# Kernel optimization log

Hardware: AMD Instinct MI355X
Metric: run time of the kernel (lower is better)

## Reference

```python
import jax, jax.numpy as jnp
import numpy as np

B, NQ, NK, D_EQUI, D_INV, D_MSG, D_FF, D_OUT = 2, 768, 768, 256, 256, 32, 128, 64


def setup_inputs() -> dict:
    key = jax.random.key(0)
    ks = jax.random.split(key, 14)
    s = 0.05  # weight init scale
    inp = {
        'q_equi': jax.random.normal(ks[0], (B, NQ, 3, D_EQUI), dtype=jnp.float32),
        'q_inv': jax.random.normal(ks[1], (B, NQ, D_INV), dtype=jnp.float32),
        'k_equi': jax.random.normal(ks[2], (B, NK, 3, D_EQUI), dtype=jnp.float32),
        'k_inv': jax.random.normal(ks[3], (B, NK, D_INV), dtype=jnp.float32),
        # projection params (stored [in, out]; torch Linear is [out, in])
        'Wqi': jax.random.normal(ks[4], (D_INV, D_MSG), dtype=jnp.float32) * s,
        'bqi': jnp.zeros((D_MSG,), jnp.float32),
        'Wki': jax.random.normal(ks[5], (D_INV, D_MSG), dtype=jnp.float32) * s,
        'bki': jnp.zeros((D_MSG,), jnp.float32),
        'Wqe': jax.random.normal(ks[6], (D_EQUI, D_MSG), dtype=jnp.float32) * s,
        'bqe': jnp.zeros((D_MSG,), jnp.float32),
        'Wke': jax.random.normal(ks[7], (D_EQUI, D_MSG), dtype=jnp.float32) * s,
        'bke': jnp.zeros((D_MSG,), jnp.float32),
        # message MLP: in_feats = 4*d_message (q_inv, k_inv, dotprods, dists)
        'W1': jax.random.normal(ks[8], (4 * D_MSG, D_FF), dtype=jnp.float32) * s,
        'b1': jnp.zeros((D_FF,), jnp.float32),
        'W2': jax.random.normal(ks[9], (D_FF, D_OUT), dtype=jnp.float32) * s,
        'b2': jnp.zeros((D_OUT,), jnp.float32),
    }
    return inp


def reference(q_equi, q_inv, k_equi, k_inv, Wqi, bqi, Wki, bki, Wqe, bqe, Wke, bke, W1, b1, W2, b2):
    b, nq = q_inv.shape[0], q_inv.shape[1]
    nk = k_inv.shape[1]
    # invariant projections -> [B, N, m]
    qi = q_inv @ Wqi + bqi
    ki = k_inv @ Wki + bki
    # equivariant projections -> [B, N, 3, m]
    qe = q_equi @ Wqe + bqe
    ke = k_equi @ Wke + bke
    # pairwise dot products over the 3D coordinate axis -> [B, Nq, Nk, m]
    dotprods = jnp.einsum('bqcm,bkcm->bqkm', qe, ke)
    # pairwise vector distances -> [B, Nq, Nk, m]
    vec = qe[:, :, None, :, :] - ke[:, None, :, :, :]  # [B, Nq, Nk, 3, m]
    dists = jnp.sqrt(jnp.sum(vec * vec, axis=3))
    feats = jnp.concatenate([
        jnp.broadcast_to(qi[:, :, None, :], (b, nq, nk, qi.shape[-1])),
        jnp.broadcast_to(ki[:, None, :, :], (b, nq, nk, ki.shape[-1])),
        dotprods,
        dists,
    ], axis=-1)  # [B, Nq, Nk, 4m]
    h = jax.nn.silu(feats @ W1 + b1)
    return h @ W2 + b2  # [B, Nq, Nk, d_out]
```

## Files before the change

kernel.cpp:

```cpp
#include <hip/hip_runtime.h>
#include <cstdint>

#define B_    2
#define NQ_   768
#define NK_   768
#define DE_   256
#define DI_   256
#define DM_   32
#define FF_   128
#define DO_   64

typedef float    f32x4 __attribute__((ext_vector_type(4)));
typedef _Float16 half8 __attribute__((ext_vector_type(8)));

__global__ __launch_bounds__(128) void node_pre(
    const float* __restrict__ inv, const float* __restrict__ equi,
    const float* __restrict__ Wi,  const float* __restrict__ bi,
    const float* __restrict__ We,  const float* __restrict__ be,
    const float* __restrict__ W1,  int w1RowOff, int addB1,
    const float* __restrict__ b1,
    float* __restrict__ e_out, float* __restrict__ sq_out, float* __restrict__ ab_out)
{
  __shared__ float inv_s[DI_];
  __shared__ float equi_s[3*DE_];
  __shared__ float qi_s[DM_];
  __shared__ float e_s[96];
  const int node = blockIdx.x;
  const int t = threadIdx.x;
  const float* invp = inv  + (size_t)node*DI_;
  const float* eqp  = equi + (size_t)node*3*DE_;
  for (int i = t; i < DI_;   i += 128) inv_s[i]  = invp[i];
  for (int i = t; i < 3*DE_; i += 128) equi_s[i] = eqp[i];
  __syncthreads();
  if (t < 96) {
    const int c = t >> 5, m = t & 31;
    const float* eq = equi_s + c*DE_;
    float a0 = be[m], a1 = 0.f, a2 = 0.f, a3 = 0.f;
    #pragma unroll 4
    for (int d = 0; d < DE_; d += 4) {
      a0 = fmaf(eq[d+0], We[(d+0)*DM_+m], a0);
      a1 = fmaf(eq[d+1], We[(d+1)*DM_+m], a1);
      a2 = fmaf(eq[d+2], We[(d+2)*DM_+m], a2);
      a3 = fmaf(eq[d+3], We[(d+3)*DM_+m], a3);
    }
    const float acc = (a0+a1)+(a2+a3);
    e_s[t] = acc;
    e_out[(size_t)node*96 + t] = acc;
  } else {
    const int m = t & 31;
    float a0 = bi[m], a1 = 0.f, a2 = 0.f, a3 = 0.f;
    #pragma unroll 4
    for (int d = 0; d < DI_; d += 4) {
      a0 = fmaf(inv_s[d+0], Wi[(d+0)*DM_+m], a0);
      a1 = fmaf(inv_s[d+1], Wi[(d+1)*DM_+m], a1);
      a2 = fmaf(inv_s[d+2], Wi[(d+2)*DM_+m], a2);
      a3 = fmaf(inv_s[d+3], Wi[(d+3)*DM_+m], a3);
    }
    qi_s[m] = (a0+a1)+(a2+a3);
  }
  __syncthreads();
  if (t < 32) {
    const float v0 = e_s[t], v1 = e_s[32+t], v2 = e_s[64+t];
    sq_out[(size_t)node*32 + t] = v0*v0 + v1*v1 + v2*v2;
  }
  float acc = addB1 ? b1[t] : 0.f;
  #pragma unroll
  for (int m = 0; m < DM_; ++m)
    acc = fmaf(qi_s[m], W1[(w1RowOff + m)*FF_ + t], acc);
  ab_out[(size_t)node*FF_ + t] = acc;
}

__global__ void pack_w(const float* __restrict__ W1, const float* __restrict__ W2,
                       _Float16* __restrict__ pk)
{
  const int i = blockIdx.x*256 + threadIdx.x;
  if (i < 8192) {
    const int j = i & 7, ln = (i>>3)&63, s = (i>>9)&1, nt = i>>10;
    const int row = 64 + s*32 + (ln>>4)*8 + j, col = nt*16 + (ln&15);
    pk[i] = (_Float16)W1[row*FF_ + col];
  } else {
    const int q = i - 8192;
    const int j = q & 7, ln = (q>>3)&63, s = (q>>9)&3, nt = q>>11;
    const int row = s*32 + (ln>>4)*8 + j, col = nt*16 + (ln&15);
    pk[i] = (_Float16)W2[row*DO_ + col];
  }
}

__global__ __launch_bounds__(256, 2) void pair_main(
    const float* __restrict__ qe_g, const float* __restrict__ ke_g,
    const float* __restrict__ qq_g, const float* __restrict__ kk_g,
    const float* __restrict__ Aq_g, const float* __restrict__ Bk_g,
    const _Float16* __restrict__ pk, const float* __restrict__ b2,
    float* __restrict__ out)
{
  __shared__ __align__(16) float    qe_s[8*100];
  __shared__ __align__(16) float    ke_s[16*100];
  __shared__ __align__(16) float    qq_s[8*36];
  __shared__ __align__(16) float    kk_s[16*36];
  __shared__ __align__(16) float    A_s[8*132];
  __shared__ __align__(16) float    B_s[16*132];
  __shared__ __align__(16) _Float16 h_s[128*136];

  const int tid = threadIdx.x;
  const int b  = blockIdx.z;
  const int q0 = blockIdx.y * 8;
  const int k0 = blockIdx.x * 16;

  { const float* p = qe_g + ((size_t)b*NQ_ + q0)*96;
    for (int i = tid; i < 8*96;  i += 256) qe_s[(i/96)*100 + (i%96)] = p[i]; }
  { const float* p = ke_g + ((size_t)b*NK_ + k0)*96;
    for (int i = tid; i < 16*96; i += 256) ke_s[(i/96)*100 + (i%96)] = p[i]; }
  { const float* p = qq_g + ((size_t)b*NQ_ + q0)*32;
    for (int i = tid; i < 8*32;  i += 256) qq_s[(i>>5)*36 + (i&31)] = p[i]; }
  { const float* p = kk_g + ((size_t)b*NK_ + k0)*32;
    for (int i = tid; i < 16*32; i += 256) kk_s[(i>>5)*36 + (i&31)] = p[i]; }
  { const float* p = Aq_g + ((size_t)b*NQ_ + q0)*128;
    for (int i = tid; i < 8*128; i += 256) A_s[(i>>7)*132 + (i&127)] = p[i]; }
  { const float* p = Bk_g + ((size_t)b*NK_ + k0)*128;
    for (int i = tid; i < 16*128; i += 256) B_s[(i>>7)*132 + (i&127)] = p[i]; }
  __syncthreads();

  const int lane = tid & 63;
  const int w    = tid >> 6;
  const int mh   = w & 1;
  const int nh   = w >> 1;
  const int n15  = lane & 15;
  const int quad = lane >> 4;
  const int mq   = quad * 8;

  const half8* pk1 = (const half8*)pk;
  half8 B1[4][2];
  #pragma unroll
  for (int nt = 0; nt < 4; ++nt)
    #pragma unroll
    for (int s = 0; s < 2; ++s)
      B1[nt][s] = pk1[(((nh*4+nt)*2 + s)<<6) + lane];

  f32x4 acc1[4][4];
  #pragma unroll
  for (int t = 0; t < 4; ++t)
    #pragma unroll
    for (int nt = 0; nt < 4; ++nt)
      acc1[t][nt] = (f32x4){0.f, 0.f, 0.f, 0.f};

  f32x4 keF[6], kkF[2];
  #pragma unroll
  for (int c = 0; c < 3; ++c) {
    keF[c*2+0] = *(const f32x4*)&ke_s[n15*100 + c*32 + mq];
    keF[c*2+1] = *(const f32x4*)&ke_s[n15*100 + c*32 + mq + 4];
  }
  kkF[0] = *(const f32x4*)&kk_s[n15*36 + mq];
  kkF[1] = *(const f32x4*)&kk_s[n15*36 + mq + 4];

  #pragma unroll
  for (int t = 0; t < 4; ++t) {
    const int qL = mh*4 + t;
    f32x4 qeF[6], qqF[2];
    #pragma unroll
    for (int c = 0; c < 3; ++c) {
      qeF[c*2+0] = *(const f32x4*)&qe_s[qL*100 + c*32 + mq];
      qeF[c*2+1] = *(const f32x4*)&qe_s[qL*100 + c*32 + mq + 4];
    }
    qqF[0] = *(const f32x4*)&qq_s[qL*36 + mq];
    qqF[1] = *(const f32x4*)&qq_s[qL*36 + mq + 4];

    half8 A0, A1;
    float dots[8];
    #pragma unroll
    for (int j = 0; j < 8; ++j) {
      const int h = j >> 2, e = j & 3;
      float d = qeF[0+h][e] * keF[0+h][e];
      d = fmaf(qeF[2+h][e], keF[2+h][e], d);
      d = fmaf(qeF[4+h][e], keF[4+h][e], d);
      dots[j] = d;
      A0[j] = (_Float16)d;
    }
    #pragma unroll
    for (int j = 0; j < 8; ++j) {
      const int h = j >> 2, e = j & 3;
      float v = qqF[h][e] + kkF[h][e] - 2.f*dots[j];
      v = fmaxf(v, 0.f);
      A1[j] = (_Float16)__builtin_sqrtf(v);
    }
    #pragma unroll
    for (int nt = 0; nt < 4; ++nt) {
      acc1[t][nt] = __builtin_amdgcn_mfma_f32_16x16x32_f16(A0, B1[nt][0], acc1[t][nt], 0, 0, 0);
      acc1[t][nt] = __builtin_amdgcn_mfma_f32_16x16x32_f16(A1, B1[nt][1], acc1[t][nt], 0, 0, 0);
    }
  }

  #pragma unroll
  for (int nt = 0; nt < 4; ++nt) {
    const int f = ((nh*4+nt)<<4) + n15;
    float Bv[4];
    #pragma unroll
    for (int r = 0; r < 4; ++r) Bv[r] = B_s[(quad*4+r)*132 + f];
    #pragma unroll
    for (int t = 0; t < 4; ++t) {
      const int qL = mh*4 + t;
      const float Av = A_s[qL*132 + f];
      #pragma unroll
      for (int r = 0; r < 4; ++r) {
        const float x = acc1[t][nt][r] + Av + Bv[r];
        const float sg = __builtin_amdgcn_rcpf(1.f + __expf(-x));
        h_s[(qL*16 + quad*4 + r)*136 + f] = (_Float16)(x * sg);
      }
    }
  }
  __syncthreads();

  const half8* pk2 = (const half8*)(pk + 8192);
  half8 B2[2][4];
  #pragma unroll
  for (int nt = 0; nt < 2; ++nt)
    #pragma unroll
    for (int s = 0; s < 4; ++s)
      B2[nt][s] = pk2[(((nh*2+nt)*4 + s)<<6) + lane];

  f32x4 acc2[4][2];
  #pragma unroll
  for (int t = 0; t < 4; ++t) { acc2[t][0] = (f32x4){0.f,0.f,0.f,0.f};
                                acc2[t][1] = (f32x4){0.f,0.f,0.f,0.f}; }
  #pragma unroll
  for (int t = 0; t < 4; ++t) {
    const int qL = mh*4 + t;
    #pragma unroll
    for (int s = 0; s < 4; ++s) {
      const half8 A2 = *(const half8*)&h_s[(qL*16 + n15)*136 + s*32 + mq];
      acc2[t][0] = __builtin_amdgcn_mfma_f32_16x16x32_f16(A2, B2[0][s], acc2[t][0], 0, 0, 0);
      acc2[t][1] = __builtin_amdgcn_mfma_f32_16x16x32_f16(A2, B2[1][s], acc2[t][1], 0, 0, 0);
    }
  }

  #pragma unroll
  for (int nt = 0; nt < 2; ++nt) {
    const int o = ((nh*2+nt)<<4) + n15;
    const float bias = b2[o];
    #pragma unroll
    for (int t = 0; t < 4; ++t) {
      const int q = q0 + mh*4 + t;
      float* op = out + (((size_t)b*NQ_ + q)*NK_ + k0 + quad*4)*DO_ + o;
      #pragma unroll
      for (int r = 0; r < 4; ++r)
        op[(size_t)r*DO_] = acc2[t][nt][r] + bias;
    }
  }
}

extern "C" void kernel_launch(void* const* d_in, const int* in_sizes, int n_in,
                              void* d_out, int out_size, void* d_ws, size_t ws_size,
                              hipStream_t stream) {
  const float* q_equi = (const float*)d_in[0];
  const float* q_inv  = (const float*)d_in[1];
  const float* k_equi = (const float*)d_in[2];
  const float* k_inv  = (const float*)d_in[3];
  const float* Wqi = (const float*)d_in[4];
  const float* bqi = (const float*)d_in[5];
  const float* Wki = (const float*)d_in[6];
  const float* bki = (const float*)d_in[7];
  const float* Wqe = (const float*)d_in[8];
  const float* bqe = (const float*)d_in[9];
  const float* Wke = (const float*)d_in[10];
  const float* bke = (const float*)d_in[11];
  const float* W1  = (const float*)d_in[12];
  const float* b1  = (const float*)d_in[13];
  const float* W2  = (const float*)d_in[14];
  const float* b2  = (const float*)d_in[15];

  float* ws = (float*)d_ws;
  float* qe = ws;
  float* ke = qe + (size_t)B_*NQ_*96;
  float* qq = ke + (size_t)B_*NK_*96;
  float* kk = qq + (size_t)B_*NQ_*32;
  float* Aq = kk + (size_t)B_*NK_*32;
  float* Bk = Aq + (size_t)B_*NQ_*128;
  _Float16* pk = (_Float16*)(Bk + (size_t)B_*NK_*128);

  node_pre<<<B_*NQ_, 128, 0, stream>>>(q_inv, q_equi, Wqi, bqi, Wqe, bqe, W1, 0, 1, b1, qe, qq, Aq);
  node_pre<<<B_*NK_, 128, 0, stream>>>(k_inv, k_equi, Wki, bki, Wke, bke, W1, 32, 0, b1, ke, kk, Bk);
  pack_w<<<64, 256, 0, stream>>>(W1, W2, pk);

  dim3 grid(NK_/16, NQ_/8, B_);
  pair_main<<<grid, 256, 0, stream>>>(qe, ke, qq, kk, Aq, Bk, pk, b2, (float*)d_out);
}
```

Baseline: 478.1 us.

## Stage pair output through LDS for vector stores and restructure warp tiling

The pair kernel now gives each warp two whole query rows across all 128 hidden features, instead of splitting the hidden and output features across warps. Because each warp only reads back its own hidden rows, the barrier between the two MLP layers can be dropped. Output tiles are written into LDS, reusing the hidden buffer, and then stored to global memory as coalesced float4 writes rather than scattered scalar stores. The sigmoid now uses exp2 directly, and the three preprocessing launches are merged into a single kernel. The cost is more weight fragments held in registers per warp and an extra LDS round trip for the output.

```diff
diff --git a/kernel.cpp b/kernel.cpp
--- a/kernel.cpp
+++ b/kernel.cpp
@@ -13,20 +13,56 @@
 typedef float    f32x4 __attribute__((ext_vector_type(4)));
 typedef _Float16 half8 __attribute__((ext_vector_type(8)));
 
-__global__ __launch_bounds__(128) void node_pre(
-    const float* __restrict__ inv, const float* __restrict__ equi,
-    const float* __restrict__ Wi,  const float* __restrict__ bi,
-    const float* __restrict__ We,  const float* __restrict__ be,
-    const float* __restrict__ W1,  int w1RowOff, int addB1,
-    const float* __restrict__ b1,
-    float* __restrict__ e_out, float* __restrict__ sq_out, float* __restrict__ ab_out)
+__global__ __launch_bounds__(128) void node_pre_all(
+    const float* __restrict__ q_inv, const float* __restrict__ q_equi,
+    const float* __restrict__ k_inv, const float* __restrict__ k_equi,
+    const float* __restrict__ Wqi, const float* __restrict__ bqi,
+    const float* __restrict__ Wki, const float* __restrict__ bki,
+    const float* __restrict__ Wqe, const float* __restrict__ bqe,
+    const float* __restrict__ Wke, const float* __restrict__ bke,
+    const float* __restrict__ W1,  const float* __restrict__ b1,
+    const float* __restrict__ W2,
+    float* __restrict__ qe, float* __restrict__ qq, float* __restrict__ Aq,
+    float* __restrict__ ke, float* __restrict__ kk, float* __restrict__ Bk,
+    _Float16* __restrict__ pk)
 {
+  const int side = blockIdx.y;
+  const int t = threadIdx.x;
+
+  if (blockIdx.x == B_*NQ_) {
+    if (side == 0) {
+      for (int i = t; i < 8192; i += 128) {
+        const int j = i & 7, ln = (i>>3)&63, s = (i>>9)&1, nt = i>>10;
+        const int row = 64 + s*32 + (ln>>4)*8 + j, col = nt*16 + (ln&15);
+        pk[i] = (_Float16)W1[row*FF_ + col];
+      }
+    } else {
+      for (int i = t; i < 8192; i += 128) {
+        const int j = i & 7, ln = (i>>3)&63, s = (i>>9)&3, nt = i>>11;
+        const int row = s*32 + (ln>>4)*8 + j, col = nt*16 + (ln&15);
+        pk[8192 + i] = (_Float16)W2[row*DO_ + col];
+      }
+    }
+    return;
+  }
+
+  const float* inv  = side ? k_inv  : q_inv;
+  const float* equi = side ? k_equi : q_equi;
+  const float* Wi   = side ? Wki : Wqi;
+  const float* bi   = side ? bki : bqi;
+  const float* We   = side ? Wke : Wqe;
+  const float* be   = side ? bke : bqe;
+  const int w1RowOff = side ? 32 : 0;
+  const int addB1    = side ? 0 : 1;
+  float* e_out  = side ? ke : qe;
+  float* sq_out = side ? kk : qq;
+  float* ab_out = side ? Bk : Aq;
+
   __shared__ float inv_s[DI_];
   __shared__ float equi_s[3*DE_];
   __shared__ float qi_s[DM_];
   __shared__ float e_s[96];
   const int node = blockIdx.x;
-  const int t = threadIdx.x;
   const float* invp = inv  + (size_t)node*DI_;
   const float* eqp  = equi + (size_t)node*3*DE_;
   for (int i = t; i < DI_;   i += 128) inv_s[i]  = invp[i];
@@ -70,22 +106,6 @@
   ab_out[(size_t)node*FF_ + t] = acc;
 }
 
-__global__ void pack_w(const float* __restrict__ W1, const float* __restrict__ W2,
-                       _Float16* __restrict__ pk)
-{
-  const int i = blockIdx.x*256 + threadIdx.x;
-  if (i < 8192) {
-    const int j = i & 7, ln = (i>>3)&63, s = (i>>9)&1, nt = i>>10;
-    const int row = 64 + s*32 + (ln>>4)*8 + j, col = nt*16 + (ln&15);
-    pk[i] = (_Float16)W1[row*FF_ + col];
-  } else {
-    const int q = i - 8192;
-    const int j = q & 7, ln = (q>>3)&63, s = (q>>9)&3, nt = q>>11;
-    const int row = s*32 + (ln>>4)*8 + j, col = nt*16 + (ln&15);
-    pk[i] = (_Float16)W2[row*DO_ + col];
-  }
-}
-
 __global__ __launch_bounds__(256, 2) void pair_main(
     const float* __restrict__ qe_g, const float* __restrict__ ke_g,
     const float* __restrict__ qq_g, const float* __restrict__ kk_g,
@@ -93,13 +113,15 @@
     const _Float16* __restrict__ pk, const float* __restrict__ b2,
     float* __restrict__ out)
 {
-  __shared__ __align__(16) float    qe_s[8*100];
-  __shared__ __align__(16) float    ke_s[16*100];
-  __shared__ __align__(16) float    qq_s[8*36];
-  __shared__ __align__(16) float    kk_s[16*36];
-  __shared__ __align__(16) float    A_s[8*132];
-  __shared__ __align__(16) float    B_s[16*132];
-  __shared__ __align__(16) _Float16 h_s[128*136];
+  __shared__ __align__(16) float qe_s[8*100];
+  __shared__ __align__(16) float ke_s[16*100];
+  __shared__ __align__(16) float qq_s[8*36];
+  __shared__ __align__(16) float kk_s[16*36];
+  __shared__ __align__(16) float A_s[8*132];
+  __shared__ __align__(16) float B_s[16*132];
+  __shared__ __align__(16) unsigned char hs_raw[128*136*2];
+  _Float16* h_s = (_Float16*)hs_raw;
+  float*    o_s = (float*)hs_raw;
 
   const int tid = threadIdx.x;
   const int b  = blockIdx.z;
@@ -122,25 +144,23 @@
 
   const int lane = tid & 63;
   const int w    = tid >> 6;
-  const int mh   = w & 1;
-  const int nh   = w >> 1;
   const int n15  = lane & 15;
   const int quad = lane >> 4;
   const int mq   = quad * 8;
 
   const half8* pk1 = (const half8*)pk;
-  half8 B1[4][2];
-  #pragma unroll
-  for (int nt = 0; nt < 4; ++nt)
+  half8 B1[8][2];
+  #pragma unroll
+  for (int nt = 0; nt < 8; ++nt)
     #pragma unroll
     for (int s = 0; s < 2; ++s)
-      B1[nt][s] = pk1[(((nh*4+nt)*2 + s)<<6) + lane];
-
-  f32x4 acc1[4][4];
-  #pragma unroll
-  for (int t = 0; t < 4; ++t)
-    #pragma unroll
-    for (int nt = 0; nt < 4; ++nt)
+      B1[nt][s] = pk1[((nt*2 + s)<<6) + lane];
+
+  f32x4 acc1[2][8];
+  #pragma unroll
+  for (int t = 0; t < 2; ++t)
+    #pragma unroll
+    for (int nt = 0; nt < 8; ++nt)
       acc1[t][nt] = (f32x4){0.f, 0.f, 0.f, 0.f};
 
   f32x4 keF[6], kkF[2];
@@ -153,8 +173,8 @@
   kkF[1] = *(const f32x4*)&kk_s[n15*36 + mq + 4];
 
   #pragma unroll
-  for (int t = 0; t < 4; ++t) {
-    const int qL = mh*4 + t;
+  for (int t = 0; t < 2; ++t) {
+    const int qL = 2*w + t;
     f32x4 qeF[6], qqF[2];
     #pragma unroll
     for (int c = 0; c < 3; ++c) {
@@ -183,67 +203,84 @@
       A1[j] = (_Float16)__builtin_sqrtf(v);
     }
     #pragma unroll
-    for (int nt = 0; nt < 4; ++nt) {
+    for (int nt = 0; nt < 8; ++nt) {
       acc1[t][nt] = __builtin_amdgcn_mfma_f32_16x16x32_f16(A0, B1[nt][0], acc1[t][nt], 0, 0, 0);
       acc1[t][nt] = __builtin_amdgcn_mfma_f32_16x16x32_f16(A1, B1[nt][1], acc1[t][nt], 0, 0, 0);
     }
   }
 
   #pragma unroll
-  for (int nt = 0; nt < 4; ++nt) {
-    const int f = ((nh*4+nt)<<4) + n15;
+  for (int nt = 0; nt < 8; ++nt) {
+    const int f = (nt<<4) + n15;
     float Bv[4];
     #pragma unroll
     for (int r = 0; r < 4; ++r) Bv[r] = B_s[(quad*4+r)*132 + f];
     #pragma unroll
-    for (int t = 0; t < 4; ++t) {
-      const int qL = mh*4 + t;
+    for (int t = 0; t < 2; ++t) {
+      const int qL = 2*w + t;
       const float Av = A_s[qL*132 + f];
       #pragma unroll
       for (int r = 0; r < 4; ++r) {
         const float x = acc1[t][nt][r] + Av + Bv[r];
-        const float sg = __builtin_amdgcn_rcpf(1.f + __expf(-x));
-        h_s[(qL*16 + quad*4 + r)*136 + f] = (_Float16)(x * sg);
+        const float e = __builtin_amdgcn_exp2f(-1.44269504f * x);
+        h_s[(qL*16 + quad*4 + r)*136 + f] = (_Float16)(x * __builtin_amdgcn_rcpf(1.f + e));
       }
     }
   }
-  __syncthreads();
 
   const half8* pk2 = (const half8*)(pk + 8192);
-  half8 B2[2][4];
-  #pragma unroll
-  for (int nt = 0; nt < 2; ++nt)
+  half8 B2[4][4];
+  #pragma unroll
+  for (int nt = 0; nt < 4; ++nt)
     #pragma unroll
     for (int s = 0; s < 4; ++s)
-      B2[nt][s] = pk2[(((nh*2+nt)*4 + s)<<6) + lane];
-
-  f32x4 acc2[4][2];
-  #pragma unroll
-  for (int t = 0; t < 4; ++t) { acc2[t][0] = (f32x4){0.f,0.f,0.f,0.f};
-                                acc2[t][1] = (f32x4){0.f,0.f,0.f,0.f}; }
-  #pragma unroll
-  for (int t = 0; t < 4; ++t) {
-    const int qL = mh*4 + t;
+      B2[nt][s] = pk2[((nt*4 + s)<<6) + lane];
+
+  f32x4 acc2[2][4];
+  #pragma unroll
+  for (int t = 0; t < 2; ++t)
+    #pragma unroll
+    for (int nt = 0; nt < 4; ++nt)
+      acc2[t][nt] = (f32x4){0.f,0.f,0.f,0.f};
+
+  #pragma unroll
+  for (int t = 0; t < 2; ++t) {
+    const int qL = 2*w + t;
     #pragma unroll
     for (int s = 0; s < 4; ++s) {
       const half8 A2 = *(const half8*)&h_s[(qL*16 + n15)*136 + s*32 + mq];
-      acc2[t][0] = __builtin_amdgcn_mfma_f32_16x16x32_f16(A2, B2[0][s], acc2[t][0], 0, 0, 0);
-      acc2[t][1] = __builtin_amdgcn_mfma_f32_16x16x32_f16(A2, B2[1][s], acc2[t][1], 0, 0, 0);
-    }
-  }
-
-  #pragma unroll
-  for (int nt = 0; nt < 2; ++nt) {
-    const int o = ((nh*2+nt)<<4) + n15;
-    const float bias = b2[o];
-    #pragma unroll
-    for (int t = 0; t < 4; ++t) {
-      const int q = q0 + mh*4 + t;
-      float* op = out + (((size_t)b*NQ_ + q)*NK_ + k0 + quad*4)*DO_ + o;
+      #pragma unroll
+      for (int nt = 0; nt < 4; ++nt)
+        acc2[t][nt] = __builtin_amdgcn_mfma_f32_16x16x32_f16(A2, B2[nt][s], acc2[t][nt], 0, 0, 0);
+    }
+  }
+
+  float bias[4];
+  #pragma unroll
+  for (int nt = 0; nt < 4; ++nt) bias[nt] = b2[(nt<<4) + n15];
+  #pragma unroll
+  for (int nt = 0; nt < 4; ++nt) {
+    const int o = (nt<<4) + n15;
+    #pragma unroll
+    for (int t = 0; t < 2; ++t) {
+      const int qL = 2*w + t;
       #pragma unroll
       for (int r = 0; r < 4; ++r)
-        op[(size_t)r*DO_] = acc2[t][nt][r] + bias;
-    }
+        o_s[(qL*16 + quad*4 + r)*68 + o] = acc2[t][nt][r] + bias[nt];
+    }
+  }
+  __syncthreads();
+
+  const size_t outBase = (((size_t)b*NQ_ + q0)*NK_ + k0)*DO_;
+  #pragma unroll
+  for (int c = 0; c < 8; ++c) {
+    const int idx  = c*256 + tid;
+    const int pair = idx >> 4;
+    const int o4   = (idx & 15) << 2;
+    const int qL   = pair >> 4;
+    const int kL   = pair & 15;
+    const f32x4 v = *(const f32x4*)&o_s[pair*68 + o4];
+    *(f32x4*)&out[outBase + ((size_t)qL*NK_ + kL)*DO_ + o4] = v;
   }
 }
 
@@ -276,9 +313,10 @@
   float* Bk = Aq + (size_t)B_*NQ_*128;
   _Float16* pk = (_Float16*)(Bk + (size_t)B_*NK_*128);
 
-  node_pre<<<B_*NQ_, 128, 0, stream>>>(q_inv, q_equi, Wqi, bqi, Wqe, bqe, W1, 0, 1, b1, qe, qq, Aq);
-  node_pre<<<B_*NK_, 128, 0, stream>>>(k_inv, k_equi, Wki, bki, Wke, bke, W1, 32, 0, b1, ke, kk, Bk);
-  pack_w<<<64, 256, 0, stream>>>(W1, W2, pk);
+  dim3 ngrid(B_*NQ_ + 1, 2);
+  node_pre_all<<<ngrid, 128, 0, stream>>>(
+      q_inv, q_equi, k_inv, k_equi, Wqi, bqi, Wki, bki, Wqe, bqe, Wke, bke,
+      W1, b1, W2, qe, qq, Aq, ke, kk, Bk, pk);
 
   dim3 grid(NK_/16, NQ_/8, B_);
   pair_main<<<grid, 256, 0, stream>>>(qe, ke, qq, kk, Aq, Bk, pk, b2, (float*)d_out);
```

New measurement: 465.4 us. 2.7% less time.
